# Kernel optimization log

Measured on AMD Instinct MI355X. Metric: run time of the kernel, lower is better.

Reference implementation:

```python
import jax, jax.numpy as jnp
import numpy as np

NUM_HEADS = 16
NUM_KV_HEADS = 4
HEAD_DIM = 128
ROPE_THETA = 500000.0
RMS_EPS = 1e-5


def _rms_norm(x, w, eps=RMS_EPS):
    # normalize over last dim in fp32, as in YuaRMSNorm
    xf = x.astype(jnp.float32)
    var = jnp.mean(xf * xf, axis=-1, keepdims=True)
    return (w * (xf * jax.lax.rsqrt(var + eps))).astype(x.dtype)


def _rotate_half(x):
    x1, x2 = jnp.split(x, 2, axis=-1)
    return jnp.concatenate([-x2, x1], axis=-1)


def _rope_cos_sin(seq_len, dim, dtype):
    inv_freq = 1.0 / (ROPE_THETA ** (jnp.arange(0, dim, 2, dtype=jnp.float32) / dim))
    pos = jnp.arange(seq_len, dtype=jnp.float32)
    freqs = pos[:, None] * inv_freq[None, :]          # [S, dim/2]
    emb = jnp.concatenate([freqs, freqs], axis=-1)     # [S, dim]
    return jnp.cos(emb).astype(dtype), jnp.sin(emb).astype(dtype)


def setup_inputs() -> dict:
    key = jax.random.key(0)
    ks = jax.random.split(key, 5)
    B, S, H = 2, 2048, 2048
    q_out = NUM_HEADS * HEAD_DIM
    kv_out = NUM_KV_HEADS * HEAD_DIM
    sc = 0.02
    return {
        "hidden_states": jax.random.normal(ks[0], (B, S, H), jnp.float32),
        "q_w": jax.random.normal(ks[1], (q_out, H), jnp.float32) * sc,
        "k_w": jax.random.normal(ks[2], (kv_out, H), jnp.float32) * sc,
        "v_w": jax.random.normal(ks[3], (kv_out, H), jnp.float32) * sc,
        "o_w": jax.random.normal(ks[4], (H, q_out), jnp.float32) * sc,
        "q_norm_w": jnp.ones((HEAD_DIM,), jnp.float32),
        "k_norm_w": jnp.ones((HEAD_DIM,), jnp.float32),
    }


def reference(hidden_states, q_w, k_w, v_w, o_w, q_norm_w, k_norm_w):
    B, S, H = hidden_states.shape
    groups = NUM_HEADS // NUM_KV_HEADS

    # fused-ish QKV projections (torch Linear: x @ W^T)
    q = jnp.einsum('bsh,oh->bso', hidden_states, q_w).reshape(B, S, NUM_HEADS, HEAD_DIM).transpose(0, 2, 1, 3)
    k = jnp.einsum('bsh,oh->bso', hidden_states, k_w).reshape(B, S, NUM_KV_HEADS, HEAD_DIM).transpose(0, 2, 1, 3)
    v = jnp.einsum('bsh,oh->bso', hidden_states, v_w).reshape(B, S, NUM_KV_HEADS, HEAD_DIM).transpose(0, 2, 1, 3)

    # QK RMSNorm over head_dim
    q = _rms_norm(q, q_norm_w)
    k = _rms_norm(k, k_norm_w)

    # RoPE (position_ids = arange(S))
    cos, sin = _rope_cos_sin(S, HEAD_DIM, q.dtype)  # [S, hd]
    cos = cos[None, None]  # [1,1,S,hd]
    sin = sin[None, None]
    q = q * cos + _rotate_half(q) * sin
    k = k * cos + _rotate_half(k) * sin

    # GQA repeat_interleave of kv heads
    k = jnp.repeat(k, groups, axis=1)  # [B, num_heads, S, hd]
    v = jnp.repeat(v, groups, axis=1)

    # causal SDPA
    scale = 1.0 / jnp.sqrt(jnp.asarray(HEAD_DIM, q.dtype))
    scores = jnp.einsum('bhqd,bhkd->bhqk', q, k) * scale
    causal = jnp.tril(jnp.ones((S, S), bool))
    scores = jnp.where(causal[None, None], scores, jnp.finfo(scores.dtype).min)
    probs = jax.nn.softmax(scores, axis=-1)
    attn = jnp.einsum('bhqk,bhkd->bhqd', probs, v)

    attn = attn.transpose(0, 2, 1, 3).reshape(B, S, NUM_HEADS * HEAD_DIM)
    return jnp.einsum('bso,ho->bsh', attn, o_w)
```

## Files before the change

### kernel.cpp

```cpp
#include <hip/hip_runtime.h>
#include <stdint.h>

#define S_LEN 2048
#define BATCH 2
#define NH 16
#define NKV 4
#define HD 128
#define HID 2048
#define MROWS (BATCH * S_LEN)

typedef unsigned short u16;
typedef __attribute__((ext_vector_type(8))) short frag_ab;
typedef __attribute__((ext_vector_type(4))) float frag_cd;

static __device__ __forceinline__ float bf2f(u16 v) {
    union { unsigned u; float f; } t; t.u = ((unsigned)v) << 16; return t.f;
}
static __device__ __forceinline__ u16 f2bf(float f) {
    union { float f; unsigned u; } t; t.f = f;
    unsigned r = t.u + 0x7fffu + ((t.u >> 16) & 1u);
    return (u16)(r >> 16);
}
static __device__ __forceinline__ void load_lds16(const u16* g, u16* l) {
    __builtin_amdgcn_global_load_lds((const __attribute__((address_space(1))) void*)g,
                                     (__attribute__((address_space(3))) void*)l, 16, 0, 0);
}

__global__ __launch_bounds__(256) void conv_f32_bf16(const float* __restrict__ src,
                                                     u16* __restrict__ dst, int n4) {
    int i = blockIdx.x * 256 + threadIdx.x;
    if (i >= n4) return;
    float4 v = ((const float4*)src)[i];
    ushort4 o;
    o.x = f2bf(v.x); o.y = f2bf(v.y); o.z = f2bf(v.z); o.w = f2bf(v.w);
    ((ushort4*)dst)[i] = o;
}

__global__ __launch_bounds__(256) void gemm_bt(const u16* __restrict__ A, const u16* __restrict__ B,
                                               float* __restrict__ C, int M, int N, int K) {
    __shared__ u16 As[128 * 32];
    __shared__ u16 Bs[128 * 32];
    const int tid = threadIdx.x;
    const int wave = tid >> 6, lane = tid & 63;
    const int quad = lane >> 4, lr = lane & 15;
    const int wm = (wave & 1) * 64, wn = (wave >> 1) * 64;
    const long bm = (long)blockIdx.x * 128, bn = (long)blockIdx.y * 128;
    const int srow = (wave << 4) + (lane >> 2);
    const int scol = (lane & 3) * 8;
    const u16* Ag = A + (bm + srow) * (long)K + scol;
    const u16* Bg = B + (bn + srow) * (long)K + scol;
    u16* AsW = As + wave * 512;
    u16* BsW = Bs + wave * 512;

    frag_cd acc[4][4];
#pragma unroll
    for (int i = 0; i < 4; i++)
#pragma unroll
        for (int j = 0; j < 4; j++) acc[i][j] = (frag_cd){0.f, 0.f, 0.f, 0.f};

    for (int k0 = 0; k0 < K; k0 += 32) {
        __syncthreads();
        load_lds16(Ag + k0, AsW);
        load_lds16(Ag + (long)64 * K + k0, AsW + 2048);
        load_lds16(Bg + k0, BsW);
        load_lds16(Bg + (long)64 * K + k0, BsW + 2048);
        __syncthreads();
        frag_ab af[4], bfr[4];
#pragma unroll
        for (int i = 0; i < 4; i++) af[i] = *(const frag_ab*)(As + (wm + i * 16 + lr) * 32 + quad * 8);
#pragma unroll
        for (int j = 0; j < 4; j++) bfr[j] = *(const frag_ab*)(Bs + (wn + j * 16 + lr) * 32 + quad * 8);
#pragma unroll
        for (int i = 0; i < 4; i++)
#pragma unroll
            for (int j = 0; j < 4; j++)
                acc[i][j] = __builtin_amdgcn_mfma_f32_16x16x32_bf16(af[i], bfr[j], acc[i][j], 0, 0, 0);
    }
#pragma unroll
    for (int i = 0; i < 4; i++)
#pragma unroll
        for (int j = 0; j < 4; j++)
#pragma unroll
            for (int r = 0; r < 4; r++) {
                long row = bm + wm + i * 16 + quad * 4 + r;
                long col = bn + wn + j * 16 + lr;
                C[row * N + col] = acc[i][j][r];
            }
}

__global__ __launch_bounds__(256) void rope_norm(const float* __restrict__ src, u16* __restrict__ dst,
                                                 const float* __restrict__ nw, int nh, int stride, int coff) {
    const int m = blockIdx.x;
    const int wave = threadIdx.x >> 6, lane = threadIdx.x & 63;
    const int s = m & (S_LEN - 1), b = m >> 11;
    const int d0 = 2 * lane;
    const float w0 = nw[d0], w1 = nw[d0 + 1];
    const int i0 = d0 & 63;
    const float lnt_over = 13.122363377404328f / 64.f;
    float inv0 = expf(-(float)i0 * lnt_over);
    float inv1 = expf(-(float)(i0 + 1) * lnt_over);
    float c0 = cosf((float)s * inv0), sn0 = sinf((float)s * inv0);
    float c1 = cosf((float)s * inv1), sn1 = sinf((float)s * inv1);
    for (int h = wave; h < nh; h += 4) {
        float2 x = *(const float2*)(src + (long)m * stride + coff + h * HD + d0);
        float ss = x.x * x.x + x.y * x.y;
#pragma unroll
        for (int off = 1; off < 64; off <<= 1) ss += __shfl_xor(ss, off);
        float rs = rsqrtf(ss * (1.f / HD) + 1e-5f);
        float xn0 = x.x * rs * w0;
        float xn1 = x.y * rs * w1;
        float p0 = __shfl_xor(xn0, 32);
        float p1 = __shfl_xor(xn1, 32);
        float r0 = (lane < 32) ? -p0 : p0;
        float r1 = (lane < 32) ? -p1 : p1;
        float y0 = xn0 * c0 + r0 * sn0;
        float y1 = xn1 * c1 + r1 * sn1;
        unsigned outw = (unsigned)f2bf(y0) | ((unsigned)f2bf(y1) << 16);
        *(unsigned*)(dst + (((long)(b * nh + h) * S_LEN + s) * HD + d0)) = outw;
    }
}

__global__ __launch_bounds__(256) void pack_vt(const float* __restrict__ src, u16* __restrict__ dst,
                                               int stride, int coff) {
    __shared__ u16 t[128 * 72];
    const int tid = threadIdx.x;
    const int st = blockIdx.x & 31;
    const int kh = (blockIdx.x >> 5) & 3;
    const int b = blockIdx.x >> 7;
    const long m0 = (long)b * S_LEN + st * 64;
#pragma unroll
    for (int c = 0; c < 8; c++) {
        int idx = c * 256 + tid;
        int r = idx >> 5, cg = idx & 31;
        float4 v = *(const float4*)(src + (m0 + r) * stride + coff + kh * HD + cg * 4);
        int col = cg * 4;
        t[(col + 0) * 72 + r] = f2bf(v.x);
        t[(col + 1) * 72 + r] = f2bf(v.y);
        t[(col + 2) * 72 + r] = f2bf(v.z);
        t[(col + 3) * 72 + r] = f2bf(v.w);
    }
    __syncthreads();
    const int d = tid >> 1, sh = (tid & 1) * 32;
    u16* dp = dst + ((long)(b * NKV + kh) * HD + d) * S_LEN + st * 64 + sh;
    const u16* tp = &t[d * 72 + sh];
    *(uint4*)(dp + 0)  = *(const uint4*)(tp + 0);
    *(uint4*)(dp + 8)  = *(const uint4*)(tp + 8);
    *(uint4*)(dp + 16) = *(const uint4*)(tp + 16);
    *(uint4*)(dp + 24) = *(const uint4*)(tp + 24);
}

__global__ __launch_bounds__(256) void flash_attn(const u16* __restrict__ Q, const u16* __restrict__ K,
                                                  const u16* __restrict__ Vt, u16* __restrict__ O) {
    __shared__ u16 Pls[4 * 32 * 80];
    const int tid = threadIdx.x;
    const int wave = tid >> 6, lane = tid & 63;
    const int quad = lane >> 4, lr = lane & 15;
    const int p = blockIdx.x & 7;
    const int h = (blockIdx.x >> 3) & 15;
    const int b = blockIdx.x >> 7;
    const int kh = h >> 2;
    const float scale = 0.08838834764831845f;
    const u16* Qb = Q + ((long)(b * NH + h) * S_LEN) * HD;
    const u16* Kb = K + ((long)(b * NKV + kh) * S_LEN) * HD;
    const u16* Vb = Vt + ((long)(b * NKV + kh) * HD) * S_LEN;
    const int pbase = wave * 32 * 80;

    for (int ph = 0; ph < 2; ph++) {
        const int t = ph ? p : (15 - p);
        const int q0 = t * 128;
        frag_ab qf[2][4];
#pragma unroll
        for (int mt = 0; mt < 2; mt++) {
            int qrow = q0 + wave * 32 + mt * 16 + lr;
#pragma unroll
            for (int ks = 0; ks < 4; ks++)
                qf[mt][ks] = *(const frag_ab*)(Qb + (long)qrow * HD + ks * 32 + quad * 8);
        }
        frag_cd oa[2][8];
        float m_i[2][4], l_i[2][4];
#pragma unroll
        for (int mt = 0; mt < 2; mt++) {
#pragma unroll
            for (int dt = 0; dt < 8; dt++) oa[mt][dt] = (frag_cd){0.f, 0.f, 0.f, 0.f};
#pragma unroll
            for (int r = 0; r < 4; r++) { m_i[mt][r] = -3e38f; l_i[mt][r] = 0.f; }
        }
        const int nkt = 2 * t + 2;

        for (int kt = 0; kt < nkt; kt++) {
            const int j0 = kt * 64;
            frag_cd sa[2][4];
#pragma unroll
            for (int mt = 0; mt < 2; mt++)
#pragma unroll
                for (int nt = 0; nt < 4; nt++) sa[mt][nt] = (frag_cd){0.f, 0.f, 0.f, 0.f};
#pragma unroll
            for (int nt = 0; nt < 4; nt++) {
                frag_ab kf[4];
#pragma unroll
                for (int ks = 0; ks < 4; ks++)
                    kf[ks] = *(const frag_ab*)(Kb + (long)(j0 + nt * 16 + lr) * HD + ks * 32 + quad * 8);
#pragma unroll
                for (int mt = 0; mt < 2; mt++)
#pragma unroll
                    for (int ks = 0; ks < 4; ks++)
                        sa[mt][nt] = __builtin_amdgcn_mfma_f32_16x16x32_bf16(qf[mt][ks], kf[ks], sa[mt][nt], 0, 0, 0);
            }

            const bool need_mask = (j0 + 63) > (q0 + wave * 32);
#pragma unroll
            for (int mt = 0; mt < 2; mt++) {
                float mrow[4] = {-3e38f, -3e38f, -3e38f, -3e38f};
#pragma unroll
                for (int nt = 0; nt < 4; nt++) {
                    int key = j0 + nt * 16 + lr;
#pragma unroll
                    for (int r = 0; r < 4; r++) {
                        int qrow = q0 + wave * 32 + mt * 16 + quad * 4 + r;
                        float v = sa[mt][nt][r] * scale;
                        if (need_mask) v = (key <= qrow) ? v : -3e38f;
                        sa[mt][nt][r] = v;
                        mrow[r] = fmaxf(mrow[r], v);
                    }
                }
#pragma unroll
                for (int off = 1; off < 16; off <<= 1)
#pragma unroll
                    for (int r = 0; r < 4; r++) mrow[r] = fmaxf(mrow[r], __shfl_xor(mrow[r], off));
                float rs[4];
#pragma unroll
                for (int r = 0; r < 4; r++) {
                    float mn = fmaxf(m_i[mt][r], mrow[r]);
                    float alpha = __expf(m_i[mt][r] - mn);
                    m_i[mt][r] = mn;
                    l_i[mt][r] *= alpha;
                    rs[r] = 0.f;
#pragma unroll
                    for (int dt = 0; dt < 8; dt++) oa[mt][dt][r] *= alpha;
                }
#pragma unroll
                for (int nt = 0; nt < 4; nt++)
#pragma unroll
                    for (int r = 0; r < 4; r++) {
                        float pw = __expf(sa[mt][nt][r] - m_i[mt][r]);
                        rs[r] += pw;
                        Pls[pbase + (mt * 16 + quad * 4 + r) * 80 + nt * 16 + lr] = f2bf(pw);
                    }
#pragma unroll
                for (int off = 1; off < 16; off <<= 1)
#pragma unroll
                    for (int r = 0; r < 4; r++) rs[r] += __shfl_xor(rs[r], off);
#pragma unroll
                for (int r = 0; r < 4; r++) l_i[mt][r] += rs[r];
            }

#pragma unroll
            for (int ks = 0; ks < 2; ks++) {
                frag_ab pf[2];
#pragma unroll
                for (int mt = 0; mt < 2; mt++)
                    pf[mt] = *(const frag_ab*)&Pls[pbase + (mt * 16 + lr) * 80 + ks * 32 + quad * 8];
                frag_ab vf[8];
#pragma unroll
                for (int dt = 0; dt < 8; dt++)
                    vf[dt] = *(const frag_ab*)(Vb + (long)(dt * 16 + lr) * S_LEN + j0 + ks * 32 + quad * 8);
#pragma unroll
                for (int dt = 0; dt < 8; dt++) {
                    oa[0][dt] = __builtin_amdgcn_mfma_f32_16x16x32_bf16(pf[0], vf[dt], oa[0][dt], 0, 0, 0);
                    oa[1][dt] = __builtin_amdgcn_mfma_f32_16x16x32_bf16(pf[1], vf[dt], oa[1][dt], 0, 0, 0);
                }
            }
        }

#pragma unroll
        for (int mt = 0; mt < 2; mt++) {
            float inv[4];
#pragma unroll
            for (int r = 0; r < 4; r++) inv[r] = 1.f / l_i[mt][r];
#pragma unroll
            for (int dt = 0; dt < 8; dt++)
#pragma unroll
                for (int r = 0; r < 4; r++) {
                    int s = q0 + wave * 32 + mt * 16 + quad * 4 + r;
                    O[((long)b * S_LEN + s) * (NH * HD) + h * HD + dt * 16 + lr] =
                        f2bf(oa[mt][dt][r] * inv[r]);
                }
        }
    }
}

extern "C" void kernel_launch(void* const* d_in, const int* in_sizes, int n_in,
                              void* d_out, int out_size, void* d_ws, size_t ws_size,
                              hipStream_t stream) {
    const float* hs  = (const float*)d_in[0];
    const float* q_w = (const float*)d_in[1];
    const float* k_w = (const float*)d_in[2];
    const float* v_w = (const float*)d_in[3];
    const float* o_w = (const float*)d_in[4];
    const float* qnw = (const float*)d_in[5];
    const float* knw = (const float*)d_in[6];
    float* out = (float*)d_out;

    char* ws = (char*)d_ws;
    u16* hs_bf  = (u16*)(ws);
    u16* wbuf   = (u16*)(ws + (16ul << 20));
    float* gout = (float*)(ws + (24ul << 20));
    u16* Kr     = (u16*)(ws + (40ul << 20));
    u16* Vt     = (u16*)(ws + (44ul << 20));
    u16* Qr     = (u16*)(ws + (56ul << 20));
    (void)ws_size; (void)in_sizes; (void)n_in; (void)out_size;

    conv_f32_bf16<<<(MROWS * HID / 4 + 255) / 256, 256, 0, stream>>>(hs, hs_bf, MROWS * HID / 4);

    conv_f32_bf16<<<(HID * HID / 4 + 255) / 256, 256, 0, stream>>>(q_w, wbuf, HID * HID / 4);
    dim3 gq(MROWS / 128, HID / 128);
    gemm_bt<<<gq, 256, 0, stream>>>(hs_bf, wbuf, gout, MROWS, HID, HID);
    rope_norm<<<MROWS, 256, 0, stream>>>(gout, Qr, qnw, NH, HID, 0);

    conv_f32_bf16<<<(NKV * HD * HID / 4 + 255) / 256, 256, 0, stream>>>(k_w, wbuf, NKV * HD * HID / 4);
    conv_f32_bf16<<<(NKV * HD * HID / 4 + 255) / 256, 256, 0, stream>>>(v_w, wbuf + NKV * HD * HID, NKV * HD * HID / 4);
    dim3 gkv(MROWS / 128, (2 * NKV * HD) / 128);
    gemm_bt<<<gkv, 256, 0, stream>>>(hs_bf, wbuf, gout, MROWS, 2 * NKV * HD, HID);
    rope_norm<<<MROWS, 256, 0, stream>>>(gout, Kr, knw, NKV, 2 * NKV * HD, 0);
    pack_vt<<<BATCH * NKV * (S_LEN / 64), 256, 0, stream>>>(gout, Vt, 2 * NKV * HD, NKV * HD);

    flash_attn<<<8 * NH * BATCH, 256, 0, stream>>>(Qr, Kr, Vt, hs_bf);

    conv_f32_bf16<<<(HID * HID / 4 + 255) / 256, 256, 0, stream>>>(o_w, wbuf, HID * HID / 4);
    gemm_bt<<<gq, 256, 0, stream>>>(hs_bf, wbuf, out, MROWS, HID, HID);
}
```

Before: 507.2 us.

## Shrink flash-attention query tile to 64 rows and launch one block per tile

The attention kernel now gives each block a single 64-row query tile, with 16 rows per wave, instead of two paired 128-row tiles. This raises the grid from 256 to 1024 blocks, and the tiles are ordered from heaviest to lightest so the causal imbalance evens out. Launch bounds now ask for 4 blocks per CU to raise occupancy. In exchange, each K/V fragment loaded from global memory feeds fewer MFMA rows, so more global traffic is needed per unit of work.

Result: slower. 585.7 us (+15.5%).

```diff
diff --git a/kernel.cpp b/kernel.cpp
--- a/kernel.cpp
+++ b/kernel.cpp
@@ -8,6 +8,7 @@
 #define HD 128
 #define HID 2048
 #define MROWS (BATCH * S_LEN)
+#define QBLK 64
 
 typedef unsigned short u16;
 typedef __attribute__((ext_vector_type(8))) short frag_ab;
@@ -149,144 +150,125 @@
     *(uint4*)(dp + 24) = *(const uint4*)(tp + 24);
 }
 
-__global__ __launch_bounds__(256) void flash_attn(const u16* __restrict__ Q, const u16* __restrict__ K,
-                                                  const u16* __restrict__ Vt, u16* __restrict__ O) {
-    __shared__ u16 Pls[4 * 32 * 80];
+__global__ __launch_bounds__(256, 4) void flash_attn(const u16* __restrict__ Q, const u16* __restrict__ K,
+                                                     const u16* __restrict__ Vt, u16* __restrict__ O) {
+    __shared__ u16 Pls[4 * 16 * 80];
     const int tid = threadIdx.x;
     const int wave = tid >> 6, lane = tid & 63;
     const int quad = lane >> 4, lr = lane & 15;
-    const int p = blockIdx.x & 7;
-    const int h = (blockIdx.x >> 3) & 15;
-    const int b = blockIdx.x >> 7;
+    const int c = blockIdx.x & 255;
+    const int g = blockIdx.x >> 8;
+    const int j = c >> 5;
+    const int bh = c & 31;
+    const int h = bh & 15, b = bh >> 4;
+    const int t = (g == 0) ? (16 + j) : (g == 1) ? (31 - j) : (g == 2) ? j : (15 - j);
     const int kh = h >> 2;
     const float scale = 0.08838834764831845f;
     const u16* Qb = Q + ((long)(b * NH + h) * S_LEN) * HD;
     const u16* Kb = K + ((long)(b * NKV + kh) * S_LEN) * HD;
     const u16* Vb = Vt + ((long)(b * NKV + kh) * HD) * S_LEN;
-    const int pbase = wave * 32 * 80;
-
-    for (int ph = 0; ph < 2; ph++) {
-        const int t = ph ? p : (15 - p);
-        const int q0 = t * 128;
-        frag_ab qf[2][4];
-#pragma unroll
-        for (int mt = 0; mt < 2; mt++) {
-            int qrow = q0 + wave * 32 + mt * 16 + lr;
+    const int pbase = wave * 16 * 80;
+
+    const int q0 = t * QBLK;
+    const int qr0 = q0 + wave * 16;
+
+    frag_ab qf[4];
+#pragma unroll
+    for (int ks = 0; ks < 4; ks++)
+        qf[ks] = *(const frag_ab*)(Qb + (long)(qr0 + lr) * HD + ks * 32 + quad * 8);
+
+    frag_cd oa[8];
+    float m_i[4], l_i[4];
+#pragma unroll
+    for (int dt = 0; dt < 8; dt++) oa[dt] = (frag_cd){0.f, 0.f, 0.f, 0.f};
+#pragma unroll
+    for (int r = 0; r < 4; r++) { m_i[r] = -3e38f; l_i[r] = 0.f; }
+
+    const int nkt = t + 1;
+    for (int kt = 0; kt < nkt; kt++) {
+        const int j0 = kt * 64;
+        frag_cd sa[4];
+#pragma unroll
+        for (int nt = 0; nt < 4; nt++) sa[nt] = (frag_cd){0.f, 0.f, 0.f, 0.f};
+#pragma unroll
+        for (int nt = 0; nt < 4; nt++) {
+            frag_ab kf[4];
 #pragma unroll
             for (int ks = 0; ks < 4; ks++)
-                qf[mt][ks] = *(const frag_ab*)(Qb + (long)qrow * HD + ks * 32 + quad * 8);
-        }
-        frag_cd oa[2][8];
-        float m_i[2][4], l_i[2][4];
-#pragma unroll
-        for (int mt = 0; mt < 2; mt++) {
-#pragma unroll
-            for (int dt = 0; dt < 8; dt++) oa[mt][dt] = (frag_cd){0.f, 0.f, 0.f, 0.f};
-#pragma unroll
-            for (int r = 0; r < 4; r++) { m_i[mt][r] = -3e38f; l_i[mt][r] = 0.f; }
-        }
-        const int nkt = 2 * t + 2;
-
-        for (int kt = 0; kt < nkt; kt++) {
-            const int j0 = kt * 64;
-            frag_cd sa[2][4];
-#pragma unroll
-            for (int mt = 0; mt < 2; mt++)
-#pragma unroll
-                for (int nt = 0; nt < 4; nt++) sa[mt][nt] = (frag_cd){0.f, 0.f, 0.f, 0.f};
-#pragma unroll
-            for (int nt = 0; nt < 4; nt++) {
-                frag_ab kf[4];
-#pragma unroll
-                for (int ks = 0; ks < 4; ks++)
-                    kf[ks] = *(const frag_ab*)(Kb + (long)(j0 + nt * 16 + lr) * HD + ks * 32 + quad * 8);
-#pragma unroll
-                for (int mt = 0; mt < 2; mt++)
-#pragma unroll
-                    for (int ks = 0; ks < 4; ks++)
-                        sa[mt][nt] = __builtin_amdgcn_mfma_f32_16x16x32_bf16(qf[mt][ks], kf[ks], sa[mt][nt], 0, 0, 0);
+                kf[ks] = *(const frag_ab*)(Kb + (long)(j0 + nt * 16 + lr) * HD + ks * 32 + quad * 8);
+#pragma unroll
+            for (int ks = 0; ks < 4; ks++)
+                sa[nt] = __builtin_amdgcn_mfma_f32_16x16x32_bf16(qf[ks], kf[ks], sa[nt], 0, 0, 0);
+        }
+
+        const bool need_mask = (j0 + 63) > qr0;
+        float mrow[4] = {-3e38f, -3e38f, -3e38f, -3e38f};
+#pragma unroll
+        for (int nt = 0; nt < 4; nt++) {
+            int key = j0 + nt * 16 + lr;
+#pragma unroll
+            for (int r = 0; r < 4; r++) {
+                int qrow = qr0 + quad * 4 + r;
+                float v = sa[nt][r] * scale;
+                if (need_mask) v = (key <= qrow) ? v : -3e38f;
+                sa[nt][r] = v;
+                mrow[r] = fmaxf(mrow[r], v);
             }
-
-            const bool need_mask = (j0 + 63) > (q0 + wave * 32);
-#pragma unroll
-            for (int mt = 0; mt < 2; mt++) {
-                float mrow[4] = {-3e38f, -3e38f, -3e38f, -3e38f};
-#pragma unroll
-                for (int nt = 0; nt < 4; nt++) {
-                    int key = j0 + nt * 16 + lr;
-#pragma unroll
-                    for (int r = 0; r < 4; r++) {
-                        int qrow = q0 + wave * 32 + mt * 16 + quad * 4 + r;
-                        float v = sa[mt][nt][r] * scale;
-                        if (need_mask) v = (key <= qrow) ? v : -3e38f;
-                        sa[mt][nt][r] = v;
-                        mrow[r] = fmaxf(mrow[r], v);
-                    }
-                }
-#pragma unroll
-                for (int off = 1; off < 16; off <<= 1)
-#pragma unroll
-                    for (int r = 0; r < 4; r++) mrow[r] = fmaxf(mrow[r], __shfl_xor(mrow[r], off));
-                float rs[4];
-#pragma unroll
-                for (int r = 0; r < 4; r++) {
-                    float mn = fmaxf(m_i[mt][r], mrow[r]);
-                    float alpha = __expf(m_i[mt][r] - mn);
-                    m_i[mt][r] = mn;
-                    l_i[mt][r] *= alpha;
-                    rs[r] = 0.f;
-#pragma unroll
-                    for (int dt = 0; dt < 8; dt++) oa[mt][dt][r] *= alpha;
-                }
-#pragma unroll
-                for (int nt = 0; nt < 4; nt++)
-#pragma unroll
-                    for (int r = 0; r < 4; r++) {
-                        float pw = __expf(sa[mt][nt][r] - m_i[mt][r]);
-                        rs[r] += pw;
-                        Pls[pbase + (mt * 16 + quad * 4 + r) * 80 + nt * 16 + lr] = f2bf(pw);
-                    }
-#pragma unroll
-                for (int off = 1; off < 16; off <<= 1)
-#pragma unroll
-                    for (int r = 0; r < 4; r++) rs[r] += __shfl_xor(rs[r], off);
-#pragma unroll
-                for (int r = 0; r < 4; r++) l_i[mt][r] += rs[r];
+        }
+#pragma unroll
+        for (int off = 1; off < 16; off <<= 1)
+#pragma unroll
+            for (int r = 0; r < 4; r++) mrow[r] = fmaxf(mrow[r], __shfl_xor(mrow[r], off));
+        float rs[4];
+#pragma unroll
+        for (int r = 0; r < 4; r++) {
+            float mn = fmaxf(m_i[r], mrow[r]);
+            float alpha = __expf(m_i[r] - mn);
+            m_i[r] = mn;
+            l_i[r] *= alpha;
+            rs[r] = 0.f;
+#pragma unroll
+            for (int dt = 0; dt < 8; dt++) oa[dt][r] *= alpha;
+        }
+#pragma unroll
+        for (int nt = 0; nt < 4; nt++)
+#pragma unroll
+            for (int r = 0; r < 4; r++) {
+                float pw = __expf(sa[nt][r] - m_i[r]);
+                rs[r] += pw;
+                Pls[pbase + (quad * 4 + r) * 80 + nt * 16 + lr] = f2bf(pw);
             }
-
-#pragma unroll
-            for (int ks = 0; ks < 2; ks++) {
-                frag_ab pf[2];
-#pragma unroll
-                for (int mt = 0; mt < 2; mt++)
-                    pf[mt] = *(const frag_ab*)&Pls[pbase + (mt * 16 + lr) * 80 + ks * 32 + quad * 8];
-                frag_ab vf[8];
-#pragma unroll
-                for (int dt = 0; dt < 8; dt++)
-                    vf[dt] = *(const frag_ab*)(Vb + (long)(dt * 16 + lr) * S_LEN + j0 + ks * 32 + quad * 8);
-#pragma unroll
-                for (int dt = 0; dt < 8; dt++) {
-                    oa[0][dt] = __builtin_amdgcn_mfma_f32_16x16x32_bf16(pf[0], vf[dt], oa[0][dt], 0, 0, 0);
-                    oa[1][dt] = __builtin_amdgcn_mfma_f32_16x16x32_bf16(pf[1], vf[dt], oa[1][dt], 0, 0, 0);
-                }
-            }
-        }
-
-#pragma unroll
-        for (int mt = 0; mt < 2; mt++) {
-            float inv[4];
-#pragma unroll
-            for (int r = 0; r < 4; r++) inv[r] = 1.f / l_i[mt][r];
+#pragma unroll
+        for (int off = 1; off < 16; off <<= 1)
+#pragma unroll
+            for (int r = 0; r < 4; r++) rs[r] += __shfl_xor(rs[r], off);
+#pragma unroll
+        for (int r = 0; r < 4; r++) l_i[r] += rs[r];
+
+#pragma unroll
+        for (int ks = 0; ks < 2; ks++) {
+            frag_ab pf = *(const frag_ab*)&Pls[pbase + lr * 80 + ks * 32 + quad * 8];
+            frag_ab vf[8];
 #pragma unroll
             for (int dt = 0; dt < 8; dt++)
-#pragma unroll
-                for (int r = 0; r < 4; r++) {
-                    int s = q0 + wave * 32 + mt * 16 + quad * 4 + r;
-                    O[((long)b * S_LEN + s) * (NH * HD) + h * HD + dt * 16 + lr] =
-                        f2bf(oa[mt][dt][r] * inv[r]);
-                }
+                vf[dt] = *(const frag_ab*)(Vb + (long)(dt * 16 + lr) * S_LEN + j0 + ks * 32 + quad * 8);
+#pragma unroll
+            for (int dt = 0; dt < 8; dt++)
+                oa[dt] = __builtin_amdgcn_mfma_f32_16x16x32_bf16(pf, vf[dt], oa[dt], 0, 0, 0);
         }
     }
+
+    float inv[4];
+#pragma unroll
+    for (int r = 0; r < 4; r++) inv[r] = 1.f / l_i[r];
+#pragma unroll
+    for (int dt = 0; dt < 8; dt++)
+#pragma unroll
+        for (int r = 0; r < 4; r++) {
+            int s = qr0 + quad * 4 + r;
+            O[((long)b * S_LEN + s) * (NH * HD) + h * HD + dt * 16 + lr] =
+                f2bf(oa[dt][r] * inv[r]);
+        }
 }
 
 extern "C" void kernel_launch(void* const* d_in, const int* in_sizes, int n_in,
@@ -324,7 +306,7 @@
     rope_norm<<<MROWS, 256, 0, stream>>>(gout, Kr, knw, NKV, 2 * NKV * HD, 0);
     pack_vt<<<BATCH * NKV * (S_LEN / 64), 256, 0, stream>>>(gout, Vt, 2 * NKV * HD, NKV * HD);
 
-    flash_attn<<<8 * NH * BATCH, 256, 0, stream>>>(Qr, Kr, Vt, hs_bf);
+    flash_attn<<<(S_LEN / QBLK) * NH * BATCH, 256, 0, stream>>>(Qr, Kr, Vt, hs_bf);
 
     conv_f32_bf16<<<(HID * HID / 4 + 255) / 256, 256, 0, stream>>>(o_w, wbuf, HID * HID / 4);
     gemm_bt<<<gq, 256, 0, stream>>>(hs_bf, wbuf, out, MROWS, HID, HID);
```

## Stage K tiles in double-buffered LDS and prefetch V fragments early

Applied to the files above, without the earlier changes.

Each K tile is now loaded once per workgroup into a padded, double-buffered LDS array, with the next tile prefetched into registers while the current one is consumed. Before, each of the four waves read the same K data from global memory on its own. V fragments for the whole 64-key tile are also issued right after QK^T, so their latency overlaps the softmax. The cost is a per-iteration __syncthreads, about 37 KB of extra LDS that can lower occupancy, and more live registers from the V prefetch.

After: 489.7 us. 1.04x faster.

```diff
diff --git a/kernel.cpp b/kernel.cpp
--- a/kernel.cpp
+++ b/kernel.cpp
@@ -8,6 +8,7 @@
 #define HD 128
 #define HID 2048
 #define MROWS (BATCH * S_LEN)
+#define KST 144
 
 typedef unsigned short u16;
 typedef __attribute__((ext_vector_type(8))) short frag_ab;
@@ -151,6 +152,7 @@
 
 __global__ __launch_bounds__(256) void flash_attn(const u16* __restrict__ Q, const u16* __restrict__ K,
                                                   const u16* __restrict__ Vt, u16* __restrict__ O) {
+    __shared__ u16 Ks[2][64 * KST];
     __shared__ u16 Pls[4 * 32 * 80];
     const int tid = threadIdx.x;
     const int wave = tid >> 6, lane = tid & 63;
@@ -164,6 +166,8 @@
     const u16* Kb = K + ((long)(b * NKV + kh) * S_LEN) * HD;
     const u16* Vb = Vt + ((long)(b * NKV + kh) * HD) * S_LEN;
     const int pbase = wave * 32 * 80;
+    const int strow = tid >> 4;
+    const int stcol = (tid & 15) * 8;
 
     for (int ph = 0; ph < 2; ph++) {
         const int t = ph ? p : (15 - p);
@@ -187,8 +191,23 @@
         }
         const int nkt = 2 * t + 2;
 
+        uint4 sreg[4];
+#pragma unroll
+        for (int cc = 0; cc < 4; cc++)
+            sreg[cc] = *(const uint4*)(Kb + (long)(cc * 16 + strow) * HD + stcol);
+#pragma unroll
+        for (int cc = 0; cc < 4; cc++)
+            *(uint4*)(&Ks[0][(cc * 16 + strow) * KST + stcol]) = sreg[cc];
+        __syncthreads();
+        int cur = 0;
+
         for (int kt = 0; kt < nkt; kt++) {
             const int j0 = kt * 64;
+            if (kt + 1 < nkt) {
+#pragma unroll
+                for (int cc = 0; cc < 4; cc++)
+                    sreg[cc] = *(const uint4*)(Kb + (long)(j0 + 64 + cc * 16 + strow) * HD + stcol);
+            }
             frag_cd sa[2][4];
 #pragma unroll
             for (int mt = 0; mt < 2; mt++)
@@ -199,13 +218,19 @@
                 frag_ab kf[4];
 #pragma unroll
                 for (int ks = 0; ks < 4; ks++)
-                    kf[ks] = *(const frag_ab*)(Kb + (long)(j0 + nt * 16 + lr) * HD + ks * 32 + quad * 8);
+                    kf[ks] = *(const frag_ab*)(&Ks[cur][(nt * 16 + lr) * KST + ks * 32 + quad * 8]);
 #pragma unroll
                 for (int mt = 0; mt < 2; mt++)
 #pragma unroll
                     for (int ks = 0; ks < 4; ks++)
                         sa[mt][nt] = __builtin_amdgcn_mfma_f32_16x16x32_bf16(qf[mt][ks], kf[ks], sa[mt][nt], 0, 0, 0);
             }
+            frag_ab vf[2][8];
+#pragma unroll
+            for (int ks = 0; ks < 2; ks++)
+#pragma unroll
+                for (int dt = 0; dt < 8; dt++)
+                    vf[ks][dt] = *(const frag_ab*)(Vb + (long)(dt * 16 + lr) * S_LEN + j0 + ks * 32 + quad * 8);
 
             const bool need_mask = (j0 + 63) > (q0 + wave * 32);
 #pragma unroll
@@ -260,16 +285,19 @@
 #pragma unroll
                 for (int mt = 0; mt < 2; mt++)
                     pf[mt] = *(const frag_ab*)&Pls[pbase + (mt * 16 + lr) * 80 + ks * 32 + quad * 8];
-                frag_ab vf[8];
-#pragma unroll
-                for (int dt = 0; dt < 8; dt++)
-                    vf[dt] = *(const frag_ab*)(Vb + (long)(dt * 16 + lr) * S_LEN + j0 + ks * 32 + quad * 8);
 #pragma unroll
                 for (int dt = 0; dt < 8; dt++) {
-                    oa[0][dt] = __builtin_amdgcn_mfma_f32_16x16x32_bf16(pf[0], vf[dt], oa[0][dt], 0, 0, 0);
-                    oa[1][dt] = __builtin_amdgcn_mfma_f32_16x16x32_bf16(pf[1], vf[dt], oa[1][dt], 0, 0, 0);
+                    oa[0][dt] = __builtin_amdgcn_mfma_f32_16x16x32_bf16(pf[0], vf[ks][dt], oa[0][dt], 0, 0, 0);
+                    oa[1][dt] = __builtin_amdgcn_mfma_f32_16x16x32_bf16(pf[1], vf[ks][dt], oa[1][dt], 0, 0, 0);
                 }
             }
+            if (kt + 1 < nkt) {
+#pragma unroll
+                for (int cc = 0; cc < 4; cc++)
+                    *(uint4*)(&Ks[cur ^ 1][(cc * 16 + strow) * KST + stcol]) = sreg[cc];
+            }
+            __syncthreads();
+            cur ^= 1;
         }
 
 #pragma unroll
```

## Split flash attention across key blocks per wave with LDS merge and finer query tiles

Applied to the files above, without the earlier changes.

Each block now handles a 32-row query tile of one head, and its four waves split the key range. Partial softmax states and outputs are merged through shared memory before writing. The block index groups the heads that share a KV head to improve cache reuse. This raises the block count to fill the GPU better, at the cost of extra LDS reduction, serialized syncs, and redundant Q loads per wave.

New measurement: 445.9 us. 1.14x faster.

```diff
diff --git a/kernel.cpp b/kernel.cpp
--- a/kernel.cpp
+++ b/kernel.cpp
@@ -149,144 +149,191 @@
     *(uint4*)(dp + 24) = *(const uint4*)(tp + 24);
 }
 
-__global__ __launch_bounds__(256) void flash_attn(const u16* __restrict__ Q, const u16* __restrict__ K,
-                                                  const u16* __restrict__ Vt, u16* __restrict__ O) {
+__global__ __launch_bounds__(256, 2) void flash_attn(const u16* __restrict__ Q, const u16* __restrict__ K,
+                                                     const u16* __restrict__ Vt, u16* __restrict__ O) {
     __shared__ u16 Pls[4 * 32 * 80];
+    __shared__ float macc[2][8][16][16];
+    __shared__ float mlb[4][2][16][2];
     const int tid = threadIdx.x;
     const int wave = tid >> 6, lane = tid & 63;
     const int quad = lane >> 4, lr = lane & 15;
-    const int p = blockIdx.x & 7;
-    const int h = (blockIdx.x >> 3) & 15;
-    const int b = blockIdx.x >> 7;
-    const int kh = h >> 2;
+    const int g = blockIdx.x & 7;
+    const int sub = (blockIdx.x >> 3) & 3;
+    const int tt = blockIdx.x >> 5;
+    const int t = 63 - tt;
+    const int b = g >> 2, kh = g & 3;
+    const int h = kh * 4 + sub;
     const float scale = 0.08838834764831845f;
     const u16* Qb = Q + ((long)(b * NH + h) * S_LEN) * HD;
     const u16* Kb = K + ((long)(b * NKV + kh) * S_LEN) * HD;
     const u16* Vb = Vt + ((long)(b * NKV + kh) * HD) * S_LEN;
     const int pbase = wave * 32 * 80;
 
-    for (int ph = 0; ph < 2; ph++) {
-        const int t = ph ? p : (15 - p);
-        const int q0 = t * 128;
-        frag_ab qf[2][4];
+    const int q0 = t * 32;
+    const int nkt = (t >> 1) + 1;
+
+    frag_ab qf[2][4];
+#pragma unroll
+    for (int mt = 0; mt < 2; mt++) {
+        int qrow = q0 + mt * 16 + lr;
+#pragma unroll
+        for (int ks = 0; ks < 4; ks++)
+            qf[mt][ks] = *(const frag_ab*)(Qb + (long)qrow * HD + ks * 32 + quad * 8);
+    }
+    frag_cd oa[2][8];
+    float m_i[2][4], l_i[2][4];
+#pragma unroll
+    for (int mt = 0; mt < 2; mt++) {
+#pragma unroll
+        for (int dt = 0; dt < 8; dt++) oa[mt][dt] = (frag_cd){0.f, 0.f, 0.f, 0.f};
+#pragma unroll
+        for (int r = 0; r < 4; r++) { m_i[mt][r] = -3e38f; l_i[mt][r] = 0.f; }
+    }
+
+    for (int kt = wave; kt < nkt; kt += 4) {
+        const int j0 = kt * 64;
+        frag_cd sa[2][4];
+#pragma unroll
+        for (int mt = 0; mt < 2; mt++)
+#pragma unroll
+            for (int nt = 0; nt < 4; nt++) sa[mt][nt] = (frag_cd){0.f, 0.f, 0.f, 0.f};
+#pragma unroll
+        for (int nt = 0; nt < 4; nt++) {
+            frag_ab kf[4];
+#pragma unroll
+            for (int ks = 0; ks < 4; ks++)
+                kf[ks] = *(const frag_ab*)(Kb + (long)(j0 + nt * 16 + lr) * HD + ks * 32 + quad * 8);
+#pragma unroll
+            for (int mt = 0; mt < 2; mt++)
+#pragma unroll
+                for (int ks = 0; ks < 4; ks++)
+                    sa[mt][nt] = __builtin_amdgcn_mfma_f32_16x16x32_bf16(qf[mt][ks], kf[ks], sa[mt][nt], 0, 0, 0);
+        }
+        frag_ab vf[2][8];
+#pragma unroll
+        for (int ks = 0; ks < 2; ks++)
+#pragma unroll
+            for (int dt = 0; dt < 8; dt++)
+                vf[ks][dt] = *(const frag_ab*)(Vb + (long)(dt * 16 + lr) * S_LEN + j0 + ks * 32 + quad * 8);
+
+        const bool need_mask = (j0 + 63) > q0;
 #pragma unroll
         for (int mt = 0; mt < 2; mt++) {
-            int qrow = q0 + wave * 32 + mt * 16 + lr;
-#pragma unroll
-            for (int ks = 0; ks < 4; ks++)
-                qf[mt][ks] = *(const frag_ab*)(Qb + (long)qrow * HD + ks * 32 + quad * 8);
-        }
-        frag_cd oa[2][8];
-        float m_i[2][4], l_i[2][4];
-#pragma unroll
-        for (int mt = 0; mt < 2; mt++) {
-#pragma unroll
-            for (int dt = 0; dt < 8; dt++) oa[mt][dt] = (frag_cd){0.f, 0.f, 0.f, 0.f};
-#pragma unroll
-            for (int r = 0; r < 4; r++) { m_i[mt][r] = -3e38f; l_i[mt][r] = 0.f; }
-        }
-        const int nkt = 2 * t + 2;
-
-        for (int kt = 0; kt < nkt; kt++) {
-            const int j0 = kt * 64;
-            frag_cd sa[2][4];
+            float mrow[4] = {-3e38f, -3e38f, -3e38f, -3e38f};
+#pragma unroll
+            for (int nt = 0; nt < 4; nt++) {
+                int key = j0 + nt * 16 + lr;
+#pragma unroll
+                for (int r = 0; r < 4; r++) {
+                    int qrow = q0 + mt * 16 + quad * 4 + r;
+                    float v = sa[mt][nt][r] * scale;
+                    if (need_mask) v = (key <= qrow) ? v : -3e38f;
+                    sa[mt][nt][r] = v;
+                    mrow[r] = fmaxf(mrow[r], v);
+                }
+            }
+#pragma unroll
+            for (int off = 1; off < 16; off <<= 1)
+#pragma unroll
+                for (int r = 0; r < 4; r++) mrow[r] = fmaxf(mrow[r], __shfl_xor(mrow[r], off));
+            float rs[4];
+#pragma unroll
+            for (int r = 0; r < 4; r++) {
+                float mn = fmaxf(m_i[mt][r], mrow[r]);
+                float alpha = __expf(m_i[mt][r] - mn);
+                m_i[mt][r] = mn;
+                l_i[mt][r] *= alpha;
+                rs[r] = 0.f;
+#pragma unroll
+                for (int dt = 0; dt < 8; dt++) oa[mt][dt][r] *= alpha;
+            }
+#pragma unroll
+            for (int nt = 0; nt < 4; nt++)
+#pragma unroll
+                for (int r = 0; r < 4; r++) {
+                    float pw = __expf(sa[mt][nt][r] - m_i[mt][r]);
+                    rs[r] += pw;
+                    Pls[pbase + (mt * 16 + quad * 4 + r) * 80 + nt * 16 + lr] = f2bf(pw);
+                }
+#pragma unroll
+            for (int off = 1; off < 16; off <<= 1)
+#pragma unroll
+                for (int r = 0; r < 4; r++) rs[r] += __shfl_xor(rs[r], off);
+#pragma unroll
+            for (int r = 0; r < 4; r++) l_i[mt][r] += rs[r];
+        }
+
+#pragma unroll
+        for (int ks = 0; ks < 2; ks++) {
+            frag_ab pf[2];
 #pragma unroll
             for (int mt = 0; mt < 2; mt++)
-#pragma unroll
-                for (int nt = 0; nt < 4; nt++) sa[mt][nt] = (frag_cd){0.f, 0.f, 0.f, 0.f};
-#pragma unroll
-            for (int nt = 0; nt < 4; nt++) {
-                frag_ab kf[4];
-#pragma unroll
-                for (int ks = 0; ks < 4; ks++)
-                    kf[ks] = *(const frag_ab*)(Kb + (long)(j0 + nt * 16 + lr) * HD + ks * 32 + quad * 8);
-#pragma unroll
-                for (int mt = 0; mt < 2; mt++)
-#pragma unroll
-                    for (int ks = 0; ks < 4; ks++)
-                        sa[mt][nt] = __builtin_amdgcn_mfma_f32_16x16x32_bf16(qf[mt][ks], kf[ks], sa[mt][nt], 0, 0, 0);
-            }
-
-            const bool need_mask = (j0 + 63) > (q0 + wave * 32);
-#pragma unroll
-            for (int mt = 0; mt < 2; mt++) {
-                float mrow[4] = {-3e38f, -3e38f, -3e38f, -3e38f};
-#pragma unroll
-                for (int nt = 0; nt < 4; nt++) {
-                    int key = j0 + nt * 16 + lr;
-#pragma unroll
-                    for (int r = 0; r < 4; r++) {
-                        int qrow = q0 + wave * 32 + mt * 16 + quad * 4 + r;
-                        float v = sa[mt][nt][r] * scale;
-                        if (need_mask) v = (key <= qrow) ? v : -3e38f;
-                        sa[mt][nt][r] = v;
-                        mrow[r] = fmaxf(mrow[r], v);
+                pf[mt] = *(const frag_ab*)&Pls[pbase + (mt * 16 + lr) * 80 + ks * 32 + quad * 8];
+#pragma unroll
+            for (int dt = 0; dt < 8; dt++) {
+                oa[0][dt] = __builtin_amdgcn_mfma_f32_16x16x32_bf16(pf[0], vf[ks][dt], oa[0][dt], 0, 0, 0);
+                oa[1][dt] = __builtin_amdgcn_mfma_f32_16x16x32_bf16(pf[1], vf[ks][dt], oa[1][dt], 0, 0, 0);
+            }
+        }
+    }
+
+    if (lr == 0) {
+#pragma unroll
+        for (int mt = 0; mt < 2; mt++)
+#pragma unroll
+            for (int r = 0; r < 4; r++) {
+                mlb[wave][mt][quad * 4 + r][0] = m_i[mt][r];
+                mlb[wave][mt][quad * 4 + r][1] = l_i[mt][r];
+            }
+    }
+    __syncthreads();
+    float inv[2][4];
+#pragma unroll
+    for (int mt = 0; mt < 2; mt++)
+#pragma unroll
+        for (int r = 0; r < 4; r++) {
+            int row = quad * 4 + r;
+            float m0 = mlb[0][mt][row][0], m1 = mlb[1][mt][row][0];
+            float m2 = mlb[2][mt][row][0], m3 = mlb[3][mt][row][0];
+            float ms = fmaxf(fmaxf(m0, m1), fmaxf(m2, m3));
+            float ls = mlb[0][mt][row][1] * __expf(m0 - ms) + mlb[1][mt][row][1] * __expf(m1 - ms)
+                     + mlb[2][mt][row][1] * __expf(m2 - ms) + mlb[3][mt][row][1] * __expf(m3 - ms);
+            inv[mt][r] = 1.f / ls;
+            float alpha = __expf(m_i[mt][r] - ms);
+#pragma unroll
+            for (int dt = 0; dt < 8; dt++) oa[mt][dt][r] *= alpha;
+        }
+    for (int w = 0; w < 4; w++) {
+        if (wave == w) {
+#pragma unroll
+            for (int mt = 0; mt < 2; mt++)
+#pragma unroll
+                for (int dt = 0; dt < 8; dt++) {
+                    frag_cd* p = (frag_cd*)&macc[mt][dt][lr][quad * 4];
+                    if (w == 0) *p = oa[mt][dt];
+                    else {
+                        frag_cd o = *p;
+#pragma unroll
+                        for (int r = 0; r < 4; r++) o[r] += oa[mt][dt][r];
+                        *p = o;
                     }
                 }
-#pragma unroll
-                for (int off = 1; off < 16; off <<= 1)
-#pragma unroll
-                    for (int r = 0; r < 4; r++) mrow[r] = fmaxf(mrow[r], __shfl_xor(mrow[r], off));
-                float rs[4];
-#pragma unroll
-                for (int r = 0; r < 4; r++) {
-                    float mn = fmaxf(m_i[mt][r], mrow[r]);
-                    float alpha = __expf(m_i[mt][r] - mn);
-                    m_i[mt][r] = mn;
-                    l_i[mt][r] *= alpha;
-                    rs[r] = 0.f;
-#pragma unroll
-                    for (int dt = 0; dt < 8; dt++) oa[mt][dt][r] *= alpha;
-                }
-#pragma unroll
-                for (int nt = 0; nt < 4; nt++)
-#pragma unroll
-                    for (int r = 0; r < 4; r++) {
-                        float pw = __expf(sa[mt][nt][r] - m_i[mt][r]);
-                        rs[r] += pw;
-                        Pls[pbase + (mt * 16 + quad * 4 + r) * 80 + nt * 16 + lr] = f2bf(pw);
-                    }
-#pragma unroll
-                for (int off = 1; off < 16; off <<= 1)
-#pragma unroll
-                    for (int r = 0; r < 4; r++) rs[r] += __shfl_xor(rs[r], off);
-#pragma unroll
-                for (int r = 0; r < 4; r++) l_i[mt][r] += rs[r];
-            }
-
-#pragma unroll
-            for (int ks = 0; ks < 2; ks++) {
-                frag_ab pf[2];
-#pragma unroll
-                for (int mt = 0; mt < 2; mt++)
-                    pf[mt] = *(const frag_ab*)&Pls[pbase + (mt * 16 + lr) * 80 + ks * 32 + quad * 8];
-                frag_ab vf[8];
-#pragma unroll
-                for (int dt = 0; dt < 8; dt++)
-                    vf[dt] = *(const frag_ab*)(Vb + (long)(dt * 16 + lr) * S_LEN + j0 + ks * 32 + quad * 8);
-#pragma unroll
-                for (int dt = 0; dt < 8; dt++) {
-                    oa[0][dt] = __builtin_amdgcn_mfma_f32_16x16x32_bf16(pf[0], vf[dt], oa[0][dt], 0, 0, 0);
-                    oa[1][dt] = __builtin_amdgcn_mfma_f32_16x16x32_bf16(pf[1], vf[dt], oa[1][dt], 0, 0, 0);
-                }
-            }
-        }
-
-#pragma unroll
-        for (int mt = 0; mt < 2; mt++) {
-            float inv[4];
-#pragma unroll
-            for (int r = 0; r < 4; r++) inv[r] = 1.f / l_i[mt][r];
-#pragma unroll
-            for (int dt = 0; dt < 8; dt++)
-#pragma unroll
-                for (int r = 0; r < 4; r++) {
-                    int s = q0 + wave * 32 + mt * 16 + quad * 4 + r;
-                    O[((long)b * S_LEN + s) * (NH * HD) + h * HD + dt * 16 + lr] =
-                        f2bf(oa[mt][dt][r] * inv[r]);
-                }
-        }
-    }
+        }
+        __syncthreads();
+    }
+#pragma unroll
+    for (int mt = 0; mt < 2; mt++)
+#pragma unroll
+        for (int dto = 0; dto < 2; dto++) {
+            int dt = wave * 2 + dto;
+            frag_cd v = *(const frag_cd*)&macc[mt][dt][lr][quad * 4];
+#pragma unroll
+            for (int r = 0; r < 4; r++) {
+                int s = q0 + mt * 16 + quad * 4 + r;
+                O[((long)b * S_LEN + s) * (NH * HD) + h * HD + dt * 16 + lr] =
+                    f2bf(v[r] * inv[mt][r]);
+            }
+        }
 }
 
 extern "C" void kernel_launch(void* const* d_in, const int* in_sizes, int n_in,
@@ -324,7 +371,7 @@
     rope_norm<<<MROWS, 256, 0, stream>>>(gout, Kr, knw, NKV, 2 * NKV * HD, 0);
     pack_vt<<<BATCH * NKV * (S_LEN / 64), 256, 0, stream>>>(gout, Vt, 2 * NKV * HD, NKV * HD);
 
-    flash_attn<<<8 * NH * BATCH, 256, 0, stream>>>(Qr, Kr, Vt, hs_bf);
+    flash_attn<<<2048, 256, 0, stream>>>(Qr, Kr, Vt, hs_bf);
 
     conv_f32_bf16<<<(HID * HID / 4 + 255) / 256, 256, 0, stream>>>(o_w, wbuf, HID * HID / 4);
     gemm_bt<<<gq, 256, 0, stream>>>(hs_bf, wbuf, out, MROWS, HID, HID);
```
